# Performance work log

Hardware: AMD Instinct MI355X
Metric: run time of the kernel (lower is better)

## Reference

```python
import jax, jax.numpy as jnp
import numpy as np

B, S, F = 256, 192, 64
HD, L, PRED = 1024, 2, 48


def setup_inputs() -> dict:
    key = jax.random.key(0)
    ks = jax.random.split(key, 9)
    s_in = 1.0 / np.sqrt(F)
    s_h = 1.0 / np.sqrt(HD)
    return {
        "x": jax.random.normal(ks[0], (B, S, F), dtype=jnp.float32),
        "W_hidden": jax.random.uniform(ks[1], (F, HD), jnp.float32, -s_in, s_in),
        "b_hidden": jax.random.uniform(ks[2], (HD,), jnp.float32, -s_in, s_in),
        "Wih": jax.random.uniform(ks[3], (L, HD, HD), jnp.float32, -s_h, s_h),
        "Whh": jax.random.uniform(ks[4], (L, HD, HD), jnp.float32, -s_h, s_h),
        "bih": jax.random.uniform(ks[5], (L, HD), jnp.float32, -s_h, s_h),
        "bhh": jax.random.uniform(ks[6], (L, HD), jnp.float32, -s_h, s_h),
        "Wo": jax.random.uniform(ks[7], (HD, F), jnp.float32, -s_h, s_h),
        "bo": jax.random.uniform(ks[8], (F,), jnp.float32, -s_h, s_h),
    }


def reference(x, W_hidden, b_hidden, Wih, Whh, bih, bhh, Wo, bo):
    # x: [B, S, F]
    x_concat = x @ W_hidden + b_hidden          # [B, S, HD]
    xs = jnp.swapaxes(x_concat, 0, 1)           # [S, B, HD] for time scan
    h0 = jnp.zeros((L, x.shape[0], HD), x.dtype)

    def step(h, x_t):
        # h: [L, B, HD], x_t: [B, HD]; standard tanh-RNN stacked layers
        inp = x_t
        new_h = []
        for l in range(L):
            hl = jnp.tanh(inp @ Wih[l] + bih[l] + h[l] @ Whh[l] + bhh[l])
            new_h.append(hl)
            inp = hl
        h_new = jnp.stack(new_h)
        return h_new, h_new[-1]

    _, ys = jax.lax.scan(step, h0, xs)           # ys: [S, B, HD] top-layer states
    # torch code stores h for t in [0, S-2] only (drops last timestep)
    H = jnp.swapaxes(ys[:-1], 0, 1)              # [B, S-1, HD]
    H = jax.nn.relu(H)
    out = H @ Wo + bo                            # [B, S-1, F]
    return out[:, -PRED:, :]
```

## Files before the change

kernel.cpp:

```cpp
#include <hip/hip_runtime.h>
#include <hip/hip_bf16.h>

#define B    256
#define S    192
#define F    64
#define HD   1024
#define PRED 48
#define TSTART (S - 1 - PRED)
#define NSLOT 48

typedef __attribute__((ext_vector_type(8))) short short8;
typedef __attribute__((ext_vector_type(4))) float f32x4;
typedef unsigned int u32;

static __device__ __forceinline__ short f2bf(float f) {
    __hip_bfloat16 h = __float2bfloat16(f);
    return *reinterpret_cast<short*>(&h);
}
static __device__ __forceinline__ f32x4 mfma16(short8 a, short8 b, f32x4 c) {
    return __builtin_amdgcn_mfma_f32_16x16x32_bf16(a, b, c, 0, 0, 0);
}
static __device__ __forceinline__ short8 ld8(const short* p) {
    return *reinterpret_cast<const short8*>(p);
}
static __device__ __forceinline__ void st_state(short* p, short v) {
    __hip_atomic_store(p, v, __ATOMIC_RELAXED, __HIP_MEMORY_SCOPE_AGENT);
}
static __device__ __forceinline__ u32 ld_flag(const u32* p) {
    return __hip_atomic_load(p, __ATOMIC_RELAXED, __HIP_MEMORY_SCOPE_AGENT);
}
static __device__ __forceinline__ void st_flag(u32* p, u32 v) {
    __hip_atomic_store(p, v, __ATOMIC_RELAXED, __HIP_MEMORY_SCOPE_AGENT);
}

__global__ void fold_kernel(const float* __restrict__ Wh,
                            const float* __restrict__ Wih0,
                            float* __restrict__ Wfold) {
    const int n = (blockIdx.x & 3) * 256 + threadIdx.x;
    const int f = blockIdx.x >> 2;
    float a = 0.f;
#pragma unroll 16
    for (int k = 0; k < HD; ++k)
        a += Wh[f * HD + k] * Wih0[(size_t)k * HD + n];
    Wfold[f * HD + n] = a;
}

__global__ void bias_kernel(const float* __restrict__ bh,
                            const float* __restrict__ Wih0,
                            const float* __restrict__ bih,
                            const float* __restrict__ bhh,
                            float* __restrict__ bf0,
                            float* __restrict__ bf1) {
    __shared__ float red[256];
    const int nl = threadIdx.x & 15;
    const int kc = threadIdx.x >> 4;
    const int n  = blockIdx.x * 16 + nl;
    float a = 0.f;
#pragma unroll 8
    for (int k = kc * 64; k < kc * 64 + 64; ++k)
        a += bh[k] * Wih0[(size_t)k * HD + n];
    red[threadIdx.x] = a;
    __syncthreads();
    if (kc == 0) {
        float s = 0.f;
#pragma unroll
        for (int j = 0; j < 16; ++j) s += red[j * 16 + nl];
        bf0[n] = s + bih[n] + bhh[n];
        bf1[n] = bih[HD + n] + bhh[HD + n];
    }
}

__global__ void transpose_cast(const float* __restrict__ src,
                               short* __restrict__ dst, int K, int N) {
    __shared__ float tile[64][65];
    const int nk = K >> 6;
    const int bk = blockIdx.x % nk;
    const int bn = blockIdx.x / nk;
    const int i  = threadIdx.x;
    {
        const int c4 = (i & 15) * 4;
        for (int it = 0; it < 4; ++it) {
            const int k = (i >> 4) + it * 16;
            const float4 v = *reinterpret_cast<const float4*>(
                &src[(size_t)(bk * 64 + k) * N + bn * 64 + c4]);
            tile[k][c4 + 0] = v.x; tile[k][c4 + 1] = v.y;
            tile[k][c4 + 2] = v.z; tile[k][c4 + 3] = v.w;
        }
    }
    __syncthreads();
    {
        const int n  = i >> 2;
        const int kb = (i & 3) * 16;
        short* dp = &dst[(size_t)(bn * 64 + n) * K + bk * 64 + kb];
#pragma unroll
        for (int j = 0; j < 16; ++j) dp[j] = f2bf(tile[kb + j][n]);
    }
}

__global__ void xcast(const float* __restrict__ x, short* __restrict__ xb) {
    const size_t i = ((size_t)blockIdx.x * 256 + threadIdx.x) * 4;
    const float4 v = *reinterpret_cast<const float4*>(&x[i]);
    short4 o;
    o.x = f2bf(v.x); o.y = f2bf(v.y); o.z = f2bf(v.z); o.w = f2bf(v.w);
    *reinterpret_cast<short4*>(&xb[i]) = o;
}

static __device__ __forceinline__ void stage1(char* lds, const short* __restrict__ src,
                                              int row0) {
    const int tid = threadIdx.x;
#pragma unroll
    for (int it = 0; it < 8; ++it) {
        const int idx = it * 512 + tid;
        const int r   = (idx >> 2) & 31;
        const int off = ((idx >> 7) << 6) + ((idx & 3) << 4);
        const f32x4 v = *reinterpret_cast<const f32x4*>(
            (const char*)src + (size_t)(row0 + r) * 2048 + off);
        *reinterpret_cast<f32x4*>(lds + (idx << 4)) = v;
    }
}

static __device__ __forceinline__ f32x4 gemmR(const char* ldsA,
                                              const short8 (&wr)[32],
                                              f32x4 acc_in) {
    f32x4 acc0 = acc_in, acc1 = {0.f,0.f,0.f,0.f};
#pragma unroll
    for (int c = 0; c < 32; ++c) {
        const short8 a = *reinterpret_cast<const short8*>(ldsA + c * 2048);
        if (c & 1) acc1 = mfma16(a, wr[c], acc1);
        else       acc0 = mfma16(a, wr[c], acc0);
    }
    return acc0 + acc1;
}

static __device__ __forceinline__ f32x4 gemmLG4(const char* ldsA,
                                                const short* __restrict__ bp,
                                                f32x4 acc_in) {
    f32x4 acc0 = acc_in, acc1 = {0.f,0.f,0.f,0.f};
    short8 b0[4], b1[4];
#pragma unroll
    for (int j = 0; j < 4; ++j) b0[j] = ld8(bp + j * 32);
#pragma unroll
    for (int c = 0; c < 8; ++c) {
        if (c < 7) {
            short8* nxt = (c & 1) ? b0 : b1;
#pragma unroll
            for (int j = 0; j < 4; ++j) nxt[j] = ld8(bp + (c + 1) * 128 + j * 32);
        }
        const short8* cur = (c & 1) ? b1 : b0;
#pragma unroll
        for (int j = 0; j < 4; ++j) {
            const short8 a = *reinterpret_cast<const short8*>(
                ldsA + (c * 4 + j) * 2048);
            if (j & 1) acc1 = mfma16(a, cur[j], acc1);
            else       acc0 = mfma16(a, cur[j], acc0);
        }
    }
    return acc0 + acc1;
}

__global__ __launch_bounds__(512, 2) void rnn_pers(
    const short* __restrict__ xbf,
    const short* __restrict__ WfoldT, const float* __restrict__ bf0,
    const short* __restrict__ WhhT0, const short* __restrict__ WihT1,
    const short* __restrict__ WhhT1, const float* __restrict__ bf1,
    short* h0h, short* h1h, u32* flags0, u32* flags1) {

    extern __shared__ char lds[];

    const int bid   = blockIdx.x;
    const int xcd   = bid & 7;
    const int u     = bid >> 3;
    const int layer = u & 1;
    const int rt    = ((xcd & 3) << 1) | ((u >> 1) & 1);
    const int ct    = ((xcd >> 2) << 3) | ((u >> 2) & 7);
    const int w     = threadIdx.x >> 6;
    const int mh    = w & 1;
    const int nq    = w >> 1;
    const int l     = threadIdx.x & 63;
    const int lr    = l & 15, kg = l >> 4;
    const int row0  = rt * 32;
    const int m0    = row0 + mh * 16;
    const int n0    = ct * 64 + nq * 16;
    const int col   = n0 + lr;
    const int rb    = m0 + kg * 4;
    const char* ldsA = lds + mh * 1024 + lr * 64 + kg * 16;

    const float bb = (layer ? bf1 : bf0)[col];
    u32* myflag = (layer ? flags1 : flags0) + (rt * 16 + ct) * 32;
    const int tid = threadIdx.x;

    short8 wr[32];
    {
        const short* wp = (layer ? WhhT1 : WhhT0) + (size_t)col * HD + kg * 8;
#pragma unroll
        for (int c = 0; c < 32; ++c) wr[c] = ld8(wp + c * 32);
    }

    if (layer == 0) {
        const short* wf = WfoldT + (size_t)col * F + kg * 8;
        const short8 wf0 = ld8(wf), wf1 = ld8(wf + 32);
        for (int k = 0; k < S - 1; ++k) {
            const short* xp = xbf + ((size_t)(m0 + lr) * S + k) * F + kg * 8;
            const short8 xa0 = ld8(xp);
            const short8 xa1 = ld8(xp + 32);
            if (k > 0) {
                __syncthreads();
                if (tid < 16) {
                    const u32* f = flags0 + (rt * 16 + tid) * 32;
                    while (ld_flag(f) < (u32)k) __builtin_amdgcn_s_sleep(1);
                } else if (tid < 32 && k >= 46) {
                    const u32* f = flags1 + (rt * 16 + (tid - 16)) * 32;
                    while (ld_flag(f) < (u32)(k - 45)) __builtin_amdgcn_s_sleep(1);
                }
                __syncthreads();
                stage1(lds, h0h + (size_t)((k - 1) % NSLOT) * B * HD, row0);
                __syncthreads();
            }
            f32x4 acc = {0.f, 0.f, 0.f, 0.f};
            acc = mfma16(xa0, wf0, acc);
            acc = mfma16(xa1, wf1, acc);
            if (k > 0) acc = gemmR(ldsA, wr, acc);
            short* hd = h0h + (size_t)(k % NSLOT) * B * HD;
#pragma unroll
            for (int r = 0; r < 4; ++r)
                st_state(&hd[(size_t)(rb + r) * HD + col],
                         f2bf(tanhf(acc[r] + bb)));
            __syncthreads();
            if (tid == 0) st_flag(myflag, (u32)(k + 1));
        }
    } else {
        if (tid == 0) st_flag(myflag, 1u);
        char* ldsBbuf = lds + 65536;
        const char* ldsB = ldsBbuf + mh * 1024 + lr * 64 + kg * 16;
        for (int k = 1; k < S; ++k) {
            const int t = k - 1;
            __syncthreads();
            if (tid < 16) {
                const u32* f = flags0 + (rt * 16 + tid) * 32;
                while (ld_flag(f) < (u32)k) __builtin_amdgcn_s_sleep(1);
            }
            __syncthreads();
            stage1(lds, h0h + (size_t)((k - 1) % NSLOT) * B * HD, row0);
            __syncthreads();
            f32x4 acc = {0.f, 0.f, 0.f, 0.f};
            acc = gemmLG4(ldsA, WihT1 + (size_t)col * HD + kg * 8, acc);
            if (t > 0) {
                if (tid < 16) {
                    const u32* f = flags1 + (rt * 16 + tid) * 32;
                    while (ld_flag(f) < (u32)k) __builtin_amdgcn_s_sleep(1);
                }
                __syncthreads();
                stage1(ldsBbuf, h1h + (size_t)((t - 1) % NSLOT) * B * HD, row0);
                __syncthreads();
                acc = gemmR(ldsB, wr, acc);
            }
#pragma unroll
            for (int r = 0; r < 4; ++r)
                st_state(&h1h[(size_t)(t % NSLOT) * B * HD
                              + (size_t)(rb + r) * HD + col],
                         f2bf(tanhf(acc[r] + bb)));
            __syncthreads();
            if (tid == 0) st_flag(myflag, (u32)(k + 1));
        }
    }
}

__global__ __launch_bounds__(256) void outgemm(
    const short* __restrict__ h1h, const short* __restrict__ WoT,
    const float* __restrict__ bo, float* __restrict__ out) {
    const int w = threadIdx.x >> 6, l = threadIdx.x & 63;
    const int lr = l & 15, kg = l >> 4;
    const int m0 = blockIdx.x * 64 + w * 16;
    const int arow = m0 + lr;
    const u32 bidx = (u32)arow / 48u;
    const u32 p    = (u32)arow % 48u;
    const u32 slot = (143u + p) % 48u;

    f32x4 acc[4] = {{0.f,0.f,0.f,0.f},{0.f,0.f,0.f,0.f},
                    {0.f,0.f,0.f,0.f},{0.f,0.f,0.f,0.f}};
    const short* ap = h1h + ((size_t)slot * B + bidx) * HD + kg * 8;
    const short* bp = WoT + (size_t)lr * HD + kg * 8;
#pragma unroll 4
    for (int k0 = 0; k0 < HD; k0 += 32) {
        short8 a = ld8(ap + k0);
#pragma unroll
        for (int j = 0; j < 8; ++j) a[j] = (a[j] < 0) ? (short)0 : a[j];
#pragma unroll
        for (int c = 0; c < 4; ++c)
            acc[c] = mfma16(a, ld8(bp + (size_t)c * 16 * HD + k0), acc[c]);
    }
    const int rb = m0 + kg * 4;
#pragma unroll
    for (int c = 0; c < 4; ++c) {
        const float bbv = bo[c * 16 + lr];
#pragma unroll
        for (int r = 0; r < 4; ++r)
            out[(size_t)(rb + r) * F + c * 16 + lr] = acc[c][r] + bbv;
    }
}

extern "C" void kernel_launch(void* const* d_in, const int* in_sizes, int n_in,
                              void* d_out, int out_size, void* d_ws, size_t ws_size,
                              hipStream_t stream) {
    const float* x   = (const float*)d_in[0];
    const float* Wh  = (const float*)d_in[1];
    const float* bh  = (const float*)d_in[2];
    const float* Wih = (const float*)d_in[3];
    const float* Whh = (const float*)d_in[4];
    const float* bih = (const float*)d_in[5];
    const float* bhh = (const float*)d_in[6];
    const float* Wo  = (const float*)d_in[7];
    const float* bo  = (const float*)d_in[8];
    float* out = (float*)d_out;

    char* p = (char*)d_ws;
    float* Wfold  = (float*)p; p += (size_t)F * HD * 4;
    float* bf0    = (float*)p; p += HD * 4;
    float* bf1    = (float*)p; p += HD * 4;
    short* WfoldT = (short*)p; p += (size_t)HD * F * 2;
    short* WhhT0  = (short*)p; p += (size_t)HD * HD * 2;
    short* WihT1  = (short*)p; p += (size_t)HD * HD * 2;
    short* WhhT1  = (short*)p; p += (size_t)HD * HD * 2;
    short* WoT    = (short*)p; p += (size_t)F * HD * 2;
    short* h0h    = (short*)p; p += (size_t)NSLOT * B * HD * 2;
    short* h1h    = (short*)p; p += (size_t)NSLOT * B * HD * 2;
    short* xbf    = (short*)p; p += (size_t)B * S * F * 2;
    u32*   sync   = (u32*)p;  p += 65536;

    hipMemsetAsync(sync, 0, 65536, stream);

    fold_kernel<<<256, 256, 0, stream>>>(Wh, Wih, Wfold);
    bias_kernel<<<64, 256, 0, stream>>>(bh, Wih, bih, bhh, bf0, bf1);
    transpose_cast<<<16, 256, 0, stream>>>(Wfold, WfoldT, F, HD);
    transpose_cast<<<256, 256, 0, stream>>>(Whh, WhhT0, HD, HD);
    transpose_cast<<<256, 256, 0, stream>>>(Wih + (size_t)HD * HD, WihT1, HD, HD);
    transpose_cast<<<256, 256, 0, stream>>>(Whh + (size_t)HD * HD, WhhT1, HD, HD);
    transpose_cast<<<16, 256, 0, stream>>>(Wo, WoT, HD, F);
    xcast<<<(B * S * F) / (256 * 4), 256, 0, stream>>>(x, xbf);

    u32* flags0 = sync;
    u32* flags1 = sync + 4096;
    void* args[] = {
        (void*)&xbf, (void*)&WfoldT, (void*)&bf0, (void*)&WhhT0,
        (void*)&WihT1, (void*)&WhhT1, (void*)&bf1,
        (void*)&h0h, (void*)&h1h, (void*)&flags0, (void*)&flags1
    };
    hipLaunchCooperativeKernel((void*)rnn_pers, dim3(256), dim3(512),
                               args, 131072, stream);

    outgemm<<<192, 256, 0, stream>>>(h1h, WoT, bo, out);
}
```

Baseline: 2.254 ms.

## Drop LDS staging and resident weights; load hidden state and weights directly from global

Removes the shared-memory staging of the previous hidden state and the register-resident recurrent weights. Each wave now loads its A fragments straight from global/L2 into registers and streams the weights the same way. Every thread polls all 16 producer flags itself, which removes most of the block-wide barriers in each step. The trade-off is more global/L2 traffic per step, because weights are re-read every timestep and A rows are loaded redundantly by the waves sharing them, plus more flag polling traffic.

Result: slower. 4.672 ms (+107.2%).

```diff
diff --git a/kernel.cpp b/kernel.cpp
--- a/kernel.cpp
+++ b/kernel.cpp
@@ -31,6 +31,17 @@
 }
 static __device__ __forceinline__ void st_flag(u32* p, u32 v) {
     __hip_atomic_store(p, v, __ATOMIC_RELAXED, __HIP_MEMORY_SCOPE_AGENT);
+}
+
+static __device__ __forceinline__ void checkflags(const u32* fb, int rt, u32 tgt) {
+    u32 fv[16];
+#pragma unroll
+    for (int i = 0; i < 16; ++i) fv[i] = ld_flag(fb + (rt * 16 + i) * 32);
+#pragma unroll
+    for (int i = 0; i < 16; ++i)
+        if (fv[i] < tgt)
+            while (ld_flag(fb + (rt * 16 + i) * 32) < tgt)
+                __builtin_amdgcn_s_sleep(1);
 }
 
 __global__ void fold_kernel(const float* __restrict__ Wh,
@@ -105,67 +116,40 @@
     *reinterpret_cast<short4*>(&xb[i]) = o;
 }
 
-static __device__ __forceinline__ void stage1(char* lds, const short* __restrict__ src,
-                                              int row0) {
-    const int tid = threadIdx.x;
-#pragma unroll
-    for (int it = 0; it < 8; ++it) {
-        const int idx = it * 512 + tid;
-        const int r   = (idx >> 2) & 31;
-        const int off = ((idx >> 7) << 6) + ((idx & 3) << 4);
-        const f32x4 v = *reinterpret_cast<const f32x4*>(
-            (const char*)src + (size_t)(row0 + r) * 2048 + off);
-        *reinterpret_cast<f32x4*>(lds + (idx << 4)) = v;
-    }
-}
-
-static __device__ __forceinline__ f32x4 gemmR(const char* ldsA,
-                                              const short8 (&wr)[32],
-                                              f32x4 acc_in) {
-    f32x4 acc0 = acc_in, acc1 = {0.f,0.f,0.f,0.f};
-#pragma unroll
-    for (int c = 0; c < 32; ++c) {
-        const short8 a = *reinterpret_cast<const short8*>(ldsA + c * 2048);
-        if (c & 1) acc1 = mfma16(a, wr[c], acc1);
-        else       acc0 = mfma16(a, wr[c], acc0);
-    }
-    return acc0 + acc1;
-}
-
-static __device__ __forceinline__ f32x4 gemmLG4(const char* ldsA,
+static __device__ __forceinline__ f32x4 gemm_du(const short* __restrict__ ap,
                                                 const short* __restrict__ bp,
                                                 f32x4 acc_in) {
-    f32x4 acc0 = acc_in, acc1 = {0.f,0.f,0.f,0.f};
+    short8 av[32];
+#pragma unroll
+    for (int c = 0; c < 32; ++c) av[c] = ld8(ap + c * 32);
+    __builtin_amdgcn_sched_barrier(0);
+    f32x4 acc0 = acc_in, acc1 = {0.f, 0.f, 0.f, 0.f};
     short8 b0[4], b1[4];
 #pragma unroll
     for (int j = 0; j < 4; ++j) b0[j] = ld8(bp + j * 32);
 #pragma unroll
-    for (int c = 0; c < 8; ++c) {
-        if (c < 7) {
-            short8* nxt = (c & 1) ? b0 : b1;
-#pragma unroll
-            for (int j = 0; j < 4; ++j) nxt[j] = ld8(bp + (c + 1) * 128 + j * 32);
-        }
-        const short8* cur = (c & 1) ? b1 : b0;
+    for (int g = 0; g < 8; ++g) {
+        if (g < 7) {
+            short8* nb = (g & 1) ? b0 : b1;
+#pragma unroll
+            for (int j = 0; j < 4; ++j) nb[j] = ld8(bp + (g + 1) * 128 + j * 32);
+        }
+        const short8* cb = (g & 1) ? b1 : b0;
 #pragma unroll
         for (int j = 0; j < 4; ++j) {
-            const short8 a = *reinterpret_cast<const short8*>(
-                ldsA + (c * 4 + j) * 2048);
-            if (j & 1) acc1 = mfma16(a, cur[j], acc1);
-            else       acc0 = mfma16(a, cur[j], acc0);
+            if (j & 1) acc1 = mfma16(av[g * 4 + j], cb[j], acc1);
+            else       acc0 = mfma16(av[g * 4 + j], cb[j], acc0);
         }
     }
     return acc0 + acc1;
 }
 
-__global__ __launch_bounds__(512, 2) void rnn_pers(
+__global__ __launch_bounds__(512) void rnn_pers(
     const short* __restrict__ xbf,
     const short* __restrict__ WfoldT, const float* __restrict__ bf0,
     const short* __restrict__ WhhT0, const short* __restrict__ WihT1,
     const short* __restrict__ WhhT1, const float* __restrict__ bf1,
     short* h0h, short* h1h, u32* flags0, u32* flags1) {
-
-    extern __shared__ char lds[];
 
     const int bid   = blockIdx.x;
     const int xcd   = bid & 7;
@@ -183,43 +167,27 @@
     const int n0    = ct * 64 + nq * 16;
     const int col   = n0 + lr;
     const int rb    = m0 + kg * 4;
-    const char* ldsA = lds + mh * 1024 + lr * 64 + kg * 16;
+    const int tid   = threadIdx.x;
 
     const float bb = (layer ? bf1 : bf0)[col];
     u32* myflag = (layer ? flags1 : flags0) + (rt * 16 + ct) * 32;
-    const int tid = threadIdx.x;
-
-    short8 wr[32];
-    {
-        const short* wp = (layer ? WhhT1 : WhhT0) + (size_t)col * HD + kg * 8;
-#pragma unroll
-        for (int c = 0; c < 32; ++c) wr[c] = ld8(wp + c * 32);
-    }
+    const size_t arow_off = (size_t)(m0 + lr) * HD + kg * 8;
 
     if (layer == 0) {
         const short* wf = WfoldT + (size_t)col * F + kg * 8;
         const short8 wf0 = ld8(wf), wf1 = ld8(wf + 32);
+        const short* whh0p = WhhT0 + (size_t)col * HD + kg * 8;
         for (int k = 0; k < S - 1; ++k) {
             const short* xp = xbf + ((size_t)(m0 + lr) * S + k) * F + kg * 8;
-            const short8 xa0 = ld8(xp);
-            const short8 xa1 = ld8(xp + 32);
+            f32x4 acc = {0.f, 0.f, 0.f, 0.f};
+            acc = mfma16(ld8(xp),      wf0, acc);
+            acc = mfma16(ld8(xp + 32), wf1, acc);
             if (k > 0) {
-                __syncthreads();
-                if (tid < 16) {
-                    const u32* f = flags0 + (rt * 16 + tid) * 32;
-                    while (ld_flag(f) < (u32)k) __builtin_amdgcn_s_sleep(1);
-                } else if (tid < 32 && k >= 46) {
-                    const u32* f = flags1 + (rt * 16 + (tid - 16)) * 32;
-                    while (ld_flag(f) < (u32)(k - 45)) __builtin_amdgcn_s_sleep(1);
-                }
-                __syncthreads();
-                stage1(lds, h0h + (size_t)((k - 1) % NSLOT) * B * HD, row0);
-                __syncthreads();
+                checkflags(flags0, rt, (u32)k);
+                acc = gemm_du(h0h + (size_t)((k - 1) % NSLOT) * B * HD + arow_off,
+                              whh0p, acc);
             }
-            f32x4 acc = {0.f, 0.f, 0.f, 0.f};
-            acc = mfma16(xa0, wf0, acc);
-            acc = mfma16(xa1, wf1, acc);
-            if (k > 0) acc = gemmR(ldsA, wr, acc);
+            if (k >= 46) checkflags(flags1, rt, (u32)(k - 45));
             short* hd = h0h + (size_t)(k % NSLOT) * B * HD;
 #pragma unroll
             for (int r = 0; r < 4; ++r)
@@ -230,34 +198,23 @@
         }
     } else {
         if (tid == 0) st_flag(myflag, 1u);
-        char* ldsBbuf = lds + 65536;
-        const char* ldsB = ldsBbuf + mh * 1024 + lr * 64 + kg * 16;
+        const short* wih1p = WihT1 + (size_t)col * HD + kg * 8;
+        const short* whh1p = WhhT1 + (size_t)col * HD + kg * 8;
         for (int k = 1; k < S; ++k) {
             const int t = k - 1;
-            __syncthreads();
-            if (tid < 16) {
-                const u32* f = flags0 + (rt * 16 + tid) * 32;
-                while (ld_flag(f) < (u32)k) __builtin_amdgcn_s_sleep(1);
+            checkflags(flags0, rt, (u32)k);
+            f32x4 acc = {0.f, 0.f, 0.f, 0.f};
+            acc = gemm_du(h0h + (size_t)((k - 1) % NSLOT) * B * HD + arow_off,
+                          wih1p, acc);
+            if (t > 0) {
+                checkflags(flags1, rt, (u32)k);
+                acc = gemm_du(h1h + (size_t)((t - 1) % NSLOT) * B * HD + arow_off,
+                              whh1p, acc);
             }
-            __syncthreads();
-            stage1(lds, h0h + (size_t)((k - 1) % NSLOT) * B * HD, row0);
-            __syncthreads();
-            f32x4 acc = {0.f, 0.f, 0.f, 0.f};
-            acc = gemmLG4(ldsA, WihT1 + (size_t)col * HD + kg * 8, acc);
-            if (t > 0) {
-                if (tid < 16) {
-                    const u32* f = flags1 + (rt * 16 + tid) * 32;
-                    while (ld_flag(f) < (u32)k) __builtin_amdgcn_s_sleep(1);
-                }
-                __syncthreads();
-                stage1(ldsBbuf, h1h + (size_t)((t - 1) % NSLOT) * B * HD, row0);
-                __syncthreads();
-                acc = gemmR(ldsB, wr, acc);
-            }
+            short* hd = h1h + (size_t)(t % NSLOT) * B * HD;
 #pragma unroll
             for (int r = 0; r < 4; ++r)
-                st_state(&h1h[(size_t)(t % NSLOT) * B * HD
-                              + (size_t)(rb + r) * HD + col],
+                st_state(&hd[(size_t)(rb + r) * HD + col],
                          f2bf(tanhf(acc[r] + bb)));
             __syncthreads();
             if (tid == 0) st_flag(myflag, (u32)(k + 1));
@@ -346,7 +303,7 @@
         (void*)&h0h, (void*)&h1h, (void*)&flags0, (void*)&flags1
     };
     hipLaunchCooperativeKernel((void*)rnn_pers, dim3(256), dim3(512),
-                               args, 131072, stream);
+                               args, 0, stream);
 
     outgemm<<<192, 256, 0, stream>>>(h1h, WoT, bo, out);
 }
```
